# Kernel optimization log

Measured on AMD Instinct MI355X. Metric: run time of the kernel, lower is better.

Reference implementation:

```python
import jax, jax.numpy as jnp
import numpy as np

HIDDEN = 2048
INNER = 1024
NUM_EXPERTS = 64
TOP_K = 8
T_TOKENS = 512


def setup_inputs() -> dict:
    key = jax.random.key(0)
    k_x, k_gw, k_gb, k_w1, k_w2 = jax.random.split(key, 5)
    x = jax.random.normal(k_x, (T_TOKENS, HIDDEN), dtype=jnp.float32)
    gate_w = jax.random.normal(k_gw, (NUM_EXPERTS, HIDDEN), dtype=jnp.float32) * 0.02
    gate_b = jax.random.normal(k_gb, (NUM_EXPERTS,), dtype=jnp.float32) * 0.02
    # fc1: fused gate+up, [E, 2*INNER, HIDDEN]; fc2: down, [E, HIDDEN, INNER]
    w1 = jax.random.normal(k_w1, (NUM_EXPERTS, 2 * INNER, HIDDEN), dtype=jnp.float32) * 0.02
    w2 = jax.random.normal(k_w2, (NUM_EXPERTS, HIDDEN, INNER), dtype=jnp.float32) * 0.02
    return {"x": x, "gate_w": gate_w, "gate_b": gate_b, "w1": w1, "w2": w2}


def reference(x, gate_w, gate_b, w1, w2):
    # Router: ReplicatedLinear with bias -> logits [T, E]
    logits = x @ gate_w.T + gate_b
    # FusedMoE default routing: softmax (fp32), top-k, renormalize
    probs = jax.nn.softmax(logits.astype(jnp.float32), axis=-1)
    topk_w, topk_idx = jax.lax.top_k(probs, TOP_K)          # [T, K]
    topk_w = topk_w / jnp.sum(topk_w, axis=-1, keepdims=True)
    T, E = probs.shape
    # Sparse combine weights scattered into a dense [T, E] matrix
    combine = jnp.zeros((T, E), dtype=topk_w.dtype)
    combine = combine.at[jnp.arange(T)[:, None], topk_idx].add(topk_w)
    # Expert MLPs (dense-over-experts reference; combine zeros out unrouted pairs)
    h = jnp.einsum('th,eih->tei', x, w1)                    # [T, E, 2*INNER]
    gate_h, up_h = h[..., :INNER], h[..., INNER:]
    act = jax.nn.gelu(gate_h, approximate=True) * up_h      # gelu_pytorch_tanh
    y = jnp.einsum('tei,ehi->teh', act, w2)                 # [T, E, HIDDEN]
    # Weighted scatter-combine back to tokens
    return jnp.einsum('te,teh->th', combine.astype(x.dtype), y)
```

## Files before the change

kernel.cpp:

```cpp
#include <hip/hip_runtime.h>
#include <hip/hip_bf16.h>

#define HIDDEN 2048
#define INNER  1024
#define NE     64
#define TOPK   8
#define NTOK   512

typedef float f32x4 __attribute__((ext_vector_type(4)));
typedef short bf16x8 __attribute__((ext_vector_type(8)));

static __device__ __forceinline__ unsigned short b16(float f) {
  return __builtin_bit_cast(unsigned short, __float2bfloat16(f));
}
static __device__ __forceinline__ unsigned int pk2(float lo, float hi) {
  return (unsigned)b16(lo) | ((unsigned)b16(hi) << 16);
}

static __device__ __forceinline__ void decode_ce32(int flat, int& c, int& e) {
  int xcd = flat & 7, s = flat >> 3;
  c = s & 31;
  e = ((s >> 5) << 3) | xcd;
}

__global__ __launch_bounds__(256) void gating_kernel(
    const float* __restrict__ x, const float* __restrict__ gw, const float* __restrict__ gb,
    int* __restrict__ ticket, int* __restrict__ counts, int* __restrict__ offsets,
    int* __restrict__ topk_e, float* __restrict__ topk_w,
    int* __restrict__ perm_tok, float* __restrict__ perm_wt,
    unsigned short* __restrict__ xb, float* __restrict__ out) {
  const int t = blockIdx.x;
  const int tid = threadIdx.x;
  const int lane = tid & 63, w = tid >> 6;

  {
    const float4* xi = (const float4*)(x + (size_t)t * HIDDEN);
    float4 v0 = xi[tid * 2], v1 = xi[tid * 2 + 1];
    ushort4 o0, o1;
    o0.x = b16(v0.x); o0.y = b16(v0.y); o0.z = b16(v0.z); o0.w = b16(v0.w);
    o1.x = b16(v1.x); o1.y = b16(v1.y); o1.z = b16(v1.z); o1.w = b16(v1.w);
    ushort4* xo = (ushort4*)(xb + (size_t)t * HIDDEN);
    xo[tid * 2] = o0; xo[tid * 2 + 1] = o1;
    f32x4 z = (f32x4)0.f;
    f32x4* orow = (f32x4*)(out + (size_t)t * HIDDEN);
    orow[tid * 2] = z; orow[tid * 2 + 1] = z;
  }

  const int e = tid >> 2, seg = tid & 3;
  const f32x4* gr = (const f32x4*)(gw + (size_t)e * HIDDEN);
  const f32x4* xr = (const f32x4*)(x + (size_t)t * HIDDEN);
  float acc = 0.f;
  #pragma unroll 8
  for (int k = 0; k < 128; ++k) {
    int idx = k * 4 + seg;
    f32x4 a = xr[idx], b = gr[idx];
    acc += a.x * b.x + a.y * b.y + a.z * b.z + a.w * b.w;
  }
  acc += __shfl_xor(acc, 1);
  acc += __shfl_xor(acc, 2);
  __shared__ float sP[NE];
  if (seg == 0) sP[e] = acc;
  __syncthreads();

  __shared__ float sW[TOPK];
  __shared__ int   sE[TOPK];
  if (w == 0) {
    float logit = gb[lane] + sP[lane];
    float m = logit;
    #pragma unroll
    for (int off = 32; off; off >>= 1) m = fmaxf(m, __shfl_xor(m, off));
    float p = __expf(logit - m);
    float s = p;
    #pragma unroll
    for (int off = 32; off; off >>= 1) s += __shfl_xor(s, off);
    p /= s;
    float myp = p;
    #pragma unroll
    for (int k = 0; k < TOPK; ++k) {
      float v = myp; int ei = lane;
      #pragma unroll
      for (int off = 32; off; off >>= 1) {
        float v2 = __shfl_xor(v, off); int e2 = __shfl_xor(ei, off);
        if (v2 > v || (v2 == v && e2 < ei)) { v = v2; ei = e2; }
      }
      if (lane == 0) { sW[k] = v; sE[k] = ei; }
      if (lane == ei) myp = -1.0f;
    }
  }
  __syncthreads();
  if (tid < TOPK) {
    float ss = 0.f;
    #pragma unroll
    for (int k = 0; k < TOPK; ++k) ss += sW[k];
    topk_e[t * TOPK + tid] = sE[tid];
    topk_w[t * TOPK + tid] = sW[tid] / ss;
  }

  __threadfence();
  __syncthreads();
  __shared__ int slast;
  if (tid == 0) {
    int old = atomicAdd(ticket, 1);
    slast = (old == (int)gridDim.x - 1);
  }
  __syncthreads();
  if (!slast) return;
  __threadfence();

  __shared__ int hcnt[NE], soff[NE], ccur[NE];
  if (tid < NE) hcnt[tid] = 0;
  __syncthreads();
  for (int i = tid; i < NTOK * TOPK; i += 256) atomicAdd(&hcnt[topk_e[i]], 1);
  __syncthreads();
  if (tid < NE) {
    int c = hcnt[tid];
    int s = c;
    #pragma unroll
    for (int off = 1; off < 64; off <<= 1) {
      int o = __shfl_up(s, off);
      if (tid >= off) s += o;
    }
    soff[tid] = s - c; ccur[tid] = 0;
    counts[tid] = c; offsets[tid] = s - c;
  }
  __syncthreads();
  for (int i = tid; i < NTOK * TOPK; i += 256) {
    int ee = topk_e[i];
    int p = atomicAdd(&ccur[ee], 1);
    int pos = soff[ee] + p;
    perm_tok[pos] = i >> 3;
    perm_wt[pos] = topk_w[i];
  }
}

__global__ __launch_bounds__(256, 4) void phase1_kernel(
    const unsigned short* __restrict__ xb, const float* __restrict__ w1,
    const int* __restrict__ offsets, const int* __restrict__ counts,
    const int* __restrict__ perm_tok, unsigned short* __restrict__ act) {
  int c, e;
  decode_ce32(blockIdx.x, c, e);
  const int n_e = counts[e];
  if (n_e == 0) return;
  const int off = offsets[e];
  const int tid = threadIdx.x;
  const int lane = tid & 63, wave = tid >> 6;
  const int u2 = lane >> 4, l15 = lane & 15;
  const int mat = wave >> 1;
  const int wm  = (wave & 1) * 64;

  const int brow = tid >> 2, bseg = tid & 3;
  const float* wg = w1 + (size_t)e * (2 * INNER) * HIDDEN;
  const float* brp = (brow < 32)
      ? wg + (size_t)(c * 32 + brow) * HIDDEN
      : wg + (size_t)(INNER + c * 32 + (brow - 32)) * HIDDEN;
  const int bslot = bseg ^ (brow & 3);

  const int arow = tid >> 1, ah = tid & 1;
  const int aslot0 = (ah * 2) ^ (arow & 3);
  const int aslot1 = (ah * 2 + 1) ^ (arow & 3);

  __shared__ uint4 smem[2][768];
  __shared__ int stok[128];
  float (*sU)[36] = (float(*)[36])&smem[0][0];

  for (int m0 = 0; m0 < n_e; m0 += 128) {
    __syncthreads();
    if (tid < 128) {
      int idx = m0 + tid;
      stok[tid] = perm_tok[off + (idx < n_e ? idx : n_e - 1)];
    }
    __syncthreads();

    const unsigned short* xrow = xb + (size_t)stok[arow] * HIDDEN;

    uint4 va0 = ((const uint4*)xrow)[ah * 2];
    uint4 va1 = ((const uint4*)xrow)[ah * 2 + 1];
    f32x4 vB0 = ((const f32x4*)brp)[bseg * 2];
    f32x4 vB1 = ((const f32x4*)brp)[bseg * 2 + 1];

    f32x4 acc[4][2];
    #pragma unroll
    for (int i = 0; i < 4; ++i)
      #pragma unroll
      for (int j = 0; j < 2; ++j) acc[i][j] = (f32x4)0.f;

    for (int k0 = 0; k0 < HIDDEN; k0 += 32) {
      const int cur = (k0 >> 5) & 1;
      uint4* A = smem[cur];
      uint4* B = smem[cur] + 512;
      A[arow * 4 + aslot0] = va0;
      A[arow * 4 + aslot1] = va1;
      B[brow * 4 + bslot] = (uint4){ pk2(vB0.x, vB0.y), pk2(vB0.z, vB0.w),
                                     pk2(vB1.x, vB1.y), pk2(vB1.z, vB1.w) };
      __syncthreads();
      int k1 = k0 + 32;
      if (k1 < HIDDEN) {
        va0 = ((const uint4*)(xrow + k1))[ah * 2];
        va1 = ((const uint4*)(xrow + k1))[ah * 2 + 1];
        vB0 = ((const f32x4*)(brp + k1))[bseg * 2];
        vB1 = ((const f32x4*)(brp + k1))[bseg * 2 + 1];
      }
      bf16x8 af[4], bfr[2];
      #pragma unroll
      for (int mi = 0; mi < 4; ++mi) {
        int r = wm + mi * 16 + l15;
        af[mi] = __builtin_bit_cast(bf16x8, A[r * 4 + (u2 ^ (r & 3))]);
      }
      #pragma unroll
      for (int ni = 0; ni < 2; ++ni) {
        int r = mat * 32 + ni * 16 + l15;
        bfr[ni] = __builtin_bit_cast(bf16x8, B[r * 4 + (u2 ^ (r & 3))]);
      }
      #pragma unroll
      for (int mi = 0; mi < 4; ++mi)
        #pragma unroll
        for (int ni = 0; ni < 2; ++ni)
          acc[mi][ni] = __builtin_amdgcn_mfma_f32_16x16x32_bf16(af[mi], bfr[ni], acc[mi][ni], 0, 0, 0);
    }

    __syncthreads();
    if (mat == 1) {
      #pragma unroll
      for (int mi = 0; mi < 4; ++mi)
        #pragma unroll
        for (int ni = 0; ni < 2; ++ni)
          #pragma unroll
          for (int r4 = 0; r4 < 4; ++r4)
            sU[wm + mi * 16 + u2 * 4 + r4][ni * 16 + l15] = acc[mi][ni][r4];
    }
    __syncthreads();
    if (mat == 0) {
      #pragma unroll
      for (int mi = 0; mi < 4; ++mi)
        #pragma unroll
        for (int r4 = 0; r4 < 4; ++r4) {
          int mrow = wm + mi * 16 + u2 * 4 + r4;
          int m = m0 + mrow;
          if (m < n_e) {
            unsigned short* arw = act + (size_t)(off + m) * INNER + c * 32;
            #pragma unroll
            for (int ni = 0; ni < 2; ++ni) {
              int col = ni * 16 + l15;
              float g = acc[mi][ni][r4];
              float uu = sU[mrow][col];
              float ge = g / (1.0f + __expf(-1.5957691216057308f * (g + 0.044715f * g * g * g)));
              arw[col] = b16(ge * uu);
            }
          }
        }
    }
  }
}

__global__ __launch_bounds__(256, 4) void phase2_kernel(
    const unsigned short* __restrict__ act, const float* __restrict__ w2,
    const int* __restrict__ offsets, const int* __restrict__ counts,
    const int* __restrict__ perm_tok, const float* __restrict__ perm_wt,
    float* __restrict__ out) {
  int c, e;
  decode_ce32(blockIdx.x, c, e);
  const int n_e = counts[e];
  if (n_e == 0) return;
  const int off = offsets[e];
  const int tid = threadIdx.x;
  const int lane = tid & 63, wave = tid >> 6;
  const int u2 = lane >> 4, l15 = lane & 15;
  const int wm = wave * 32;

  const int brow = tid >> 2, bseg = tid & 3;
  const float* brp = w2 + ((size_t)e * HIDDEN + c * 64 + brow) * INNER;
  const int bslot = bseg ^ (brow & 3);

  const int arow = tid >> 1, ah = tid & 1;
  const int aslot0 = (ah * 2) ^ (arow & 3);
  const int aslot1 = (ah * 2 + 1) ^ (arow & 3);

  __shared__ uint4 smem[2][768];
  __shared__ int   stok[128];
  __shared__ float swt[128];

  for (int m0 = 0; m0 < n_e; m0 += 128) {
    __syncthreads();
    if (tid < 128) {
      int idx = m0 + tid;
      int cl = idx < n_e ? idx : n_e - 1;
      stok[tid] = perm_tok[off + cl];
      swt[tid] = (idx < n_e) ? perm_wt[off + cl] : 0.f;
    }
    __syncthreads();

    const unsigned short* arp = act + (size_t)(off + (m0 + arow < n_e ? m0 + arow : n_e - 1)) * INNER;

    uint4 va0 = ((const uint4*)arp)[ah * 2];
    uint4 va1 = ((const uint4*)arp)[ah * 2 + 1];
    f32x4 vB0 = ((const f32x4*)brp)[bseg * 2];
    f32x4 vB1 = ((const f32x4*)brp)[bseg * 2 + 1];

    f32x4 acc[2][4];
    #pragma unroll
    for (int i = 0; i < 2; ++i)
      #pragma unroll
      for (int j = 0; j < 4; ++j) acc[i][j] = (f32x4)0.f;

    for (int k0 = 0; k0 < INNER; k0 += 32) {
      const int cur = (k0 >> 5) & 1;
      uint4* A = smem[cur];
      uint4* B = smem[cur] + 512;
      A[arow * 4 + aslot0] = va0;
      A[arow * 4 + aslot1] = va1;
      B[brow * 4 + bslot] = (uint4){ pk2(vB0.x, vB0.y), pk2(vB0.z, vB0.w),
                                     pk2(vB1.x, vB1.y), pk2(vB1.z, vB1.w) };
      __syncthreads();
      int k1 = k0 + 32;
      if (k1 < INNER) {
        va0 = ((const uint4*)(arp + k1))[ah * 2];
        va1 = ((const uint4*)(arp + k1))[ah * 2 + 1];
        vB0 = ((const f32x4*)(brp + k1))[bseg * 2];
        vB1 = ((const f32x4*)(brp + k1))[bseg * 2 + 1];
      }
      bf16x8 af[2], bfr[4];
      #pragma unroll
      for (int mi = 0; mi < 2; ++mi) {
        int r = wm + mi * 16 + l15;
        af[mi] = __builtin_bit_cast(bf16x8, A[r * 4 + (u2 ^ (r & 3))]);
      }
      #pragma unroll
      for (int ni = 0; ni < 4; ++ni) {
        int r = ni * 16 + l15;
        bfr[ni] = __builtin_bit_cast(bf16x8, B[r * 4 + (u2 ^ (r & 3))]);
      }
      #pragma unroll
      for (int mi = 0; mi < 2; ++mi)
        #pragma unroll
        for (int ni = 0; ni < 4; ++ni)
          acc[mi][ni] = __builtin_amdgcn_mfma_f32_16x16x32_bf16(af[mi], bfr[ni], acc[mi][ni], 0, 0, 0);
    }

    #pragma unroll
    for (int mi = 0; mi < 2; ++mi)
      #pragma unroll
      for (int r4 = 0; r4 < 4; ++r4) {
        int mrow = wm + mi * 16 + u2 * 4 + r4;
        int m = m0 + mrow;
        if (m < n_e) {
          int tok = stok[mrow];
          float wt = swt[mrow];
          float* orow = out + (size_t)tok * HIDDEN + c * 64;
          #pragma unroll
          for (int ni = 0; ni < 4; ++ni)
            atomicAdd(&orow[ni * 16 + l15], wt * acc[mi][ni][r4]);
        }
      }
    __syncthreads();
  }
}

extern "C" void kernel_launch(void* const* d_in, const int* in_sizes, int n_in,
                              void* d_out, int out_size, void* d_ws, size_t ws_size,
                              hipStream_t stream) {
  const float* x  = (const float*)d_in[0];
  const float* gw = (const float*)d_in[1];
  const float* gb = (const float*)d_in[2];
  const float* w1 = (const float*)d_in[3];
  const float* w2 = (const float*)d_in[4];
  float* out = (float*)d_out;

  char* ws = (char*)d_ws;
  int*   ticket   = (int*)(ws + 0x000);
  int*   counts   = (int*)(ws + 0x100);
  int*   offsets  = (int*)(ws + 0x200);
  int*   topk_e   = (int*)(ws + 0x1000);
  float* topk_w   = (float*)(ws + 0x5000);
  int*   perm_tok = (int*)(ws + 0x9000);
  float* perm_wt  = (float*)(ws + 0xD000);
  unsigned short* xb  = (unsigned short*)(ws + 0x11000);
  unsigned short* act = (unsigned short*)(ws + 0x220000);

  hipMemsetAsync(ticket, 0, 0x40, stream);

  gating_kernel<<<NTOK, 256, 0, stream>>>(x, gw, gb, ticket, counts, offsets,
                                          topk_e, topk_w, perm_tok, perm_wt, xb, out);
  phase1_kernel<<<2048, 256, 0, stream>>>(xb, w1, offsets, counts, perm_tok, act);
  phase2_kernel<<<2048, 256, 0, stream>>>(act, w2, offsets, counts, perm_tok, perm_wt, out);
}
```

Measured before the change: 479.8 us.

## Stage expert GEMM tiles via direct global-to-LDS loads with BK=64

Both expert GEMM kernels now use global_load_lds to copy A (bf16 activations) and B (fp32 weights) tiles straight into shared memory, using XOR-swizzled addresses and a K step of 64. The fp32-to-bf16 conversion of weights moves from the staging path to the fragment-read path. LDS per block grows and the occupancy hint drops from 4 to 2 blocks per CU. The aim is to free registers and VALU work in the load path and to overlap the next tile's fetch with the current MFMAs. In exchange, fp32 weights take twice the LDS space, and each wave redundantly converts B fragments on every read.

```diff
diff --git a/kernel.cpp b/kernel.cpp
--- a/kernel.cpp
+++ b/kernel.cpp
@@ -15,6 +15,11 @@
 }
 static __device__ __forceinline__ unsigned int pk2(float lo, float hi) {
   return (unsigned)b16(lo) | ((unsigned)b16(hi) << 16);
+}
+static __device__ __forceinline__ void gload16(const void* g, void* l) {
+  __builtin_amdgcn_global_load_lds(
+      (const __attribute__((address_space(1))) unsigned int*)g,
+      (__attribute__((address_space(3))) unsigned int*)l, 16, 0, 0);
 }
 
 static __device__ __forceinline__ void decode_ce32(int flat, int& c, int& e) {
@@ -133,7 +138,7 @@
   }
 }
 
-__global__ __launch_bounds__(256, 4) void phase1_kernel(
+__global__ __launch_bounds__(256, 2) void phase1_kernel(
     const unsigned short* __restrict__ xb, const float* __restrict__ w1,
     const int* __restrict__ offsets, const int* __restrict__ counts,
     const int* __restrict__ perm_tok, unsigned short* __restrict__ act) {
@@ -148,20 +153,29 @@
   const int mat = wave >> 1;
   const int wm  = (wave & 1) * 64;
 
-  const int brow = tid >> 2, bseg = tid & 3;
   const float* wg = w1 + (size_t)e * (2 * INNER) * HIDDEN;
-  const float* brp = (brow < 32)
-      ? wg + (size_t)(c * 32 + brow) * HIDDEN
-      : wg + (size_t)(INNER + c * 32 + (brow - 32)) * HIDDEN;
-  const int bslot = bseg ^ (brow & 3);
-
-  const int arow = tid >> 1, ah = tid & 1;
-  const int aslot0 = (ah * 2) ^ (arow & 3);
-  const int aslot1 = (ah * 2 + 1) ^ (arow & 3);
-
-  __shared__ uint4 smem[2][768];
+  const float* bptr[4];
+  #pragma unroll
+  for (int j = 0; j < 4; ++j) {
+    int brow = j * 16 + wave * 4 + (lane >> 4);
+    const float* base = (brow < 32)
+        ? wg + (size_t)(c * 32 + brow) * HIDDEN
+        : wg + (size_t)(INNER + c * 32 + (brow - 32)) * HIDDEN;
+    bptr[j] = base + (((lane & 15) ^ (brow & 15)) << 2);
+  }
+
+  __shared__ uint4 smem[2][2048];
   __shared__ int stok[128];
   float (*sU)[36] = (float(*)[36])&smem[0][0];
+
+#define STAGE1(CUR, K0)                                                       \
+  {                                                                           \
+    _Pragma("unroll")                                                         \
+    for (int j = 0; j < 4; ++j) {                                             \
+      gload16(aptr[j] + (K0), &smem[CUR][(j * 32 + wave * 8) * 8]);           \
+      gload16(bptr[j] + (K0), &smem[CUR][1024 + (j * 16 + wave * 4) * 16]);   \
+    }                                                                         \
+  }
 
   for (int m0 = 0; m0 < n_e; m0 += 128) {
     __syncthreads();
@@ -171,12 +185,12 @@
     }
     __syncthreads();
 
-    const unsigned short* xrow = xb + (size_t)stok[arow] * HIDDEN;
-
-    uint4 va0 = ((const uint4*)xrow)[ah * 2];
-    uint4 va1 = ((const uint4*)xrow)[ah * 2 + 1];
-    f32x4 vB0 = ((const f32x4*)brp)[bseg * 2];
-    f32x4 vB1 = ((const f32x4*)brp)[bseg * 2 + 1];
+    const unsigned short* aptr[4];
+    #pragma unroll
+    for (int j = 0; j < 4; ++j) {
+      int row = j * 32 + wave * 8 + (lane >> 3);
+      aptr[j] = xb + (size_t)stok[row] * HIDDEN + (((lane & 7) ^ (row & 7)) << 3);
+    }
 
     f32x4 acc[4][2];
     #pragma unroll
@@ -184,41 +198,40 @@
       #pragma unroll
       for (int j = 0; j < 2; ++j) acc[i][j] = (f32x4)0.f;
 
-    for (int k0 = 0; k0 < HIDDEN; k0 += 32) {
-      const int cur = (k0 >> 5) & 1;
-      uint4* A = smem[cur];
-      uint4* B = smem[cur] + 512;
-      A[arow * 4 + aslot0] = va0;
-      A[arow * 4 + aslot1] = va1;
-      B[brow * 4 + bslot] = (uint4){ pk2(vB0.x, vB0.y), pk2(vB0.z, vB0.w),
-                                     pk2(vB1.x, vB1.y), pk2(vB1.z, vB1.w) };
+    STAGE1(0, 0)
+    __syncthreads();
+
+    for (int k0 = 0; k0 < HIDDEN; k0 += 64) {
+      const int cur = (k0 >> 6) & 1;
+      if (k0 + 64 < HIDDEN) STAGE1(cur ^ 1, k0 + 64)
+      const uint4* A  = smem[cur];
+      const uint4* Bq = smem[cur] + 1024;
+      #pragma unroll
+      for (int ks = 0; ks < 2; ++ks) {
+        const int u = ks * 4 + u2;
+        bf16x8 af[4], bfr[2];
+        #pragma unroll
+        for (int mi = 0; mi < 4; ++mi) {
+          int r = wm + mi * 16 + l15;
+          af[mi] = __builtin_bit_cast(bf16x8, A[r * 8 + (u ^ (r & 7))]);
+        }
+        #pragma unroll
+        for (int ni = 0; ni < 2; ++ni) {
+          int rb = (mat * 32 + ni * 16 + l15) * 16;
+          f32x4 p0 = __builtin_bit_cast(f32x4, Bq[rb + ((2 * u) ^ l15)]);
+          f32x4 p1 = __builtin_bit_cast(f32x4, Bq[rb + ((2 * u + 1) ^ l15)]);
+          uint4 uu = { pk2(p0.x, p0.y), pk2(p0.z, p0.w), pk2(p1.x, p1.y), pk2(p1.z, p1.w) };
+          bfr[ni] = __builtin_bit_cast(bf16x8, uu);
+        }
+        #pragma unroll
+        for (int mi = 0; mi < 4; ++mi)
+          #pragma unroll
+          for (int ni = 0; ni < 2; ++ni)
+            acc[mi][ni] = __builtin_amdgcn_mfma_f32_16x16x32_bf16(af[mi], bfr[ni], acc[mi][ni], 0, 0, 0);
+      }
       __syncthreads();
-      int k1 = k0 + 32;
-      if (k1 < HIDDEN) {
-        va0 = ((const uint4*)(xrow + k1))[ah * 2];
-        va1 = ((const uint4*)(xrow + k1))[ah * 2 + 1];
-        vB0 = ((const f32x4*)(brp + k1))[bseg * 2];
-        vB1 = ((const f32x4*)(brp + k1))[bseg * 2 + 1];
-      }
-      bf16x8 af[4], bfr[2];
-      #pragma unroll
-      for (int mi = 0; mi < 4; ++mi) {
-        int r = wm + mi * 16 + l15;
-        af[mi] = __builtin_bit_cast(bf16x8, A[r * 4 + (u2 ^ (r & 3))]);
-      }
-      #pragma unroll
-      for (int ni = 0; ni < 2; ++ni) {
-        int r = mat * 32 + ni * 16 + l15;
-        bfr[ni] = __builtin_bit_cast(bf16x8, B[r * 4 + (u2 ^ (r & 3))]);
-      }
-      #pragma unroll
-      for (int mi = 0; mi < 4; ++mi)
-        #pragma unroll
-        for (int ni = 0; ni < 2; ++ni)
-          acc[mi][ni] = __builtin_amdgcn_mfma_f32_16x16x32_bf16(af[mi], bfr[ni], acc[mi][ni], 0, 0, 0);
-    }
-
-    __syncthreads();
+    }
+
     if (mat == 1) {
       #pragma unroll
       for (int mi = 0; mi < 4; ++mi)
@@ -250,9 +263,10 @@
         }
     }
   }
-}
-
-__global__ __launch_bounds__(256, 4) void phase2_kernel(
+#undef STAGE1
+}
+
+__global__ __launch_bounds__(256, 2) void phase2_kernel(
     const unsigned short* __restrict__ act, const float* __restrict__ w2,
     const int* __restrict__ offsets, const int* __restrict__ counts,
     const int* __restrict__ perm_tok, const float* __restrict__ perm_wt,
@@ -267,17 +281,26 @@
   const int u2 = lane >> 4, l15 = lane & 15;
   const int wm = wave * 32;
 
-  const int brow = tid >> 2, bseg = tid & 3;
-  const float* brp = w2 + ((size_t)e * HIDDEN + c * 64 + brow) * INNER;
-  const int bslot = bseg ^ (brow & 3);
-
-  const int arow = tid >> 1, ah = tid & 1;
-  const int aslot0 = (ah * 2) ^ (arow & 3);
-  const int aslot1 = (ah * 2 + 1) ^ (arow & 3);
-
-  __shared__ uint4 smem[2][768];
+  const float* bptr[4];
+  #pragma unroll
+  for (int j = 0; j < 4; ++j) {
+    int brow = j * 16 + wave * 4 + (lane >> 4);
+    bptr[j] = w2 + ((size_t)e * HIDDEN + c * 64 + brow) * INNER
+            + (((lane & 15) ^ (brow & 15)) << 2);
+  }
+
+  __shared__ uint4 smem[2][2048];
   __shared__ int   stok[128];
   __shared__ float swt[128];
+
+#define STAGE2(CUR, K0)                                                       \
+  {                                                                           \
+    _Pragma("unroll")                                                         \
+    for (int j = 0; j < 4; ++j) {                                             \
+      gload16(aptr[j] + (K0), &smem[CUR][(j * 32 + wave * 8) * 8]);           \
+      gload16(bptr[j] + (K0), &smem[CUR][1024 + (j * 16 + wave * 4) * 16]);   \
+    }                                                                         \
+  }
 
   for (int m0 = 0; m0 < n_e; m0 += 128) {
     __syncthreads();
@@ -289,12 +312,14 @@
     }
     __syncthreads();
 
-    const unsigned short* arp = act + (size_t)(off + (m0 + arow < n_e ? m0 + arow : n_e - 1)) * INNER;
-
-    uint4 va0 = ((const uint4*)arp)[ah * 2];
-    uint4 va1 = ((const uint4*)arp)[ah * 2 + 1];
-    f32x4 vB0 = ((const f32x4*)brp)[bseg * 2];
-    f32x4 vB1 = ((const f32x4*)brp)[bseg * 2 + 1];
+    const unsigned short* aptr[4];
+    #pragma unroll
+    for (int j = 0; j < 4; ++j) {
+      int row = j * 32 + wave * 8 + (lane >> 3);
+      int m = m0 + row;
+      aptr[j] = act + (size_t)(off + (m < n_e ? m : n_e - 1)) * INNER
+              + (((lane & 7) ^ (row & 7)) << 3);
+    }
 
     f32x4 acc[2][4];
     #pragma unroll
@@ -302,38 +327,38 @@
       #pragma unroll
       for (int j = 0; j < 4; ++j) acc[i][j] = (f32x4)0.f;
 
-    for (int k0 = 0; k0 < INNER; k0 += 32) {
-      const int cur = (k0 >> 5) & 1;
-      uint4* A = smem[cur];
-      uint4* B = smem[cur] + 512;
-      A[arow * 4 + aslot0] = va0;
-      A[arow * 4 + aslot1] = va1;
-      B[brow * 4 + bslot] = (uint4){ pk2(vB0.x, vB0.y), pk2(vB0.z, vB0.w),
-                                     pk2(vB1.x, vB1.y), pk2(vB1.z, vB1.w) };
+    STAGE2(0, 0)
+    __syncthreads();
+
+    for (int k0 = 0; k0 < INNER; k0 += 64) {
+      const int cur = (k0 >> 6) & 1;
+      if (k0 + 64 < INNER) STAGE2(cur ^ 1, k0 + 64)
+      const uint4* A  = smem[cur];
+      const uint4* Bq = smem[cur] + 1024;
+      #pragma unroll
+      for (int ks = 0; ks < 2; ++ks) {
+        const int u = ks * 4 + u2;
+        bf16x8 af[2], bfr[4];
+        #pragma unroll
+        for (int mi = 0; mi < 2; ++mi) {
+          int r = wm + mi * 16 + l15;
+          af[mi] = __builtin_bit_cast(bf16x8, A[r * 8 + (u ^ (r & 7))]);
+        }
+        #pragma unroll
+        for (int ni = 0; ni < 4; ++ni) {
+          int rb = (ni * 16 + l15) * 16;
+          f32x4 p0 = __builtin_bit_cast(f32x4, Bq[rb + ((2 * u) ^ l15)]);
+          f32x4 p1 = __builtin_bit_cast(f32x4, Bq[rb + ((2 * u + 1) ^ l15)]);
+          uint4 uu = { pk2(p0.x, p0.y), pk2(p0.z, p0.w), pk2(p1.x, p1.y), pk2(p1.z, p1.w) };
+          bfr[ni] = __builtin_bit_cast(bf16x8, uu);
+        }
+        #pragma unroll
+        for (int mi = 0; mi < 2; ++mi)
+          #pragma unroll
+          for (int ni = 0; ni < 4; ++ni)
+            acc[mi][ni] = __builtin_amdgcn_mfma_f32_16x16x32_bf16(af[mi], bfr[ni], acc[mi][ni], 0, 0, 0);
+      }
       __syncthreads();
-      int k1 = k0 + 32;
-      if (k1 < INNER) {
-        va0 = ((const uint4*)(arp + k1))[ah * 2];
-        va1 = ((const uint4*)(arp + k1))[ah * 2 + 1];
-        vB0 = ((const f32x4*)(brp + k1))[bseg * 2];
-        vB1 = ((const f32x4*)(brp + k1))[bseg * 2 + 1];
-      }
-      bf16x8 af[2], bfr[4];
-      #pragma unroll
-      for (int mi = 0; mi < 2; ++mi) {
-        int r = wm + mi * 16 + l15;
-        af[mi] = __builtin_bit_cast(bf16x8, A[r * 4 + (u2 ^ (r & 3))]);
-      }
-      #pragma unroll
-      for (int ni = 0; ni < 4; ++ni) {
-        int r = ni * 16 + l15;
-        bfr[ni] = __builtin_bit_cast(bf16x8, B[r * 4 + (u2 ^ (r & 3))]);
-      }
-      #pragma unroll
-      for (int mi = 0; mi < 2; ++mi)
-        #pragma unroll
-        for (int ni = 0; ni < 4; ++ni)
-          acc[mi][ni] = __builtin_amdgcn_mfma_f32_16x16x32_bf16(af[mi], bfr[ni], acc[mi][ni], 0, 0, 0);
     }
 
     #pragma unroll
@@ -351,8 +376,8 @@
             atomicAdd(&orow[ni * 16 + l15], wt * acc[mi][ni][r4]);
         }
       }
-    __syncthreads();
-  }
+  }
+#undef STAGE2
 }
 
 extern "C" void kernel_launch(void* const* d_in, const int* in_sizes, int n_in,
```

Result: faster. 444.2 us (-7.4%).
